# Kernel optimization log

Measured on AMD Instinct MI355X. Metric: run time of the kernel, lower is better.

The kernel has to match this reference:

```python
import jax, jax.numpy as jnp
import numpy as np

K = 128
HEADS = 8

def setup_inputs() -> dict:
    key = jax.random.key(0)
    ks = jax.random.split(key, 6)
    B, S = 4, 2048
    x = jax.random.normal(ks[0], (B, S, K), dtype=jnp.float32)
    sc = 1.0 / np.sqrt(K)
    Wq = jax.random.normal(ks[1], (K, K * HEADS), dtype=jnp.float32) * sc
    Wk = jax.random.normal(ks[2], (K, K * HEADS), dtype=jnp.float32) * sc
    Wv = jax.random.normal(ks[3], (K, K * HEADS), dtype=jnp.float32) * sc
    Wo = jax.random.normal(ks[4], (HEADS * K, K), dtype=jnp.float32) * (1.0 / np.sqrt(HEADS * K))
    bo = jnp.zeros((K,), dtype=jnp.float32)
    return {"x": x, "Wq": Wq, "Wk": Wk, "Wv": Wv, "Wo": Wo, "bo": bo}

def reference(x, Wq, Wk, Wv, Wo, bo):
    B, S, k = x.shape
    h = HEADS
    # projections: (B,S,k) @ (k, k*h) -> (B,S,h,k) -> (B,h,S,k)
    q = (x @ Wq).reshape(B, S, h, k).transpose(0, 2, 1, 3)
    kk = (x @ Wk).reshape(B, S, h, k).transpose(0, 2, 1, 3)
    v = (x @ Wv).reshape(B, S, h, k).transpose(0, 2, 1, 3)
    scale = k ** -0.25
    q = q * scale
    kk = kk * scale
    scores = jnp.einsum('bhqd,bhkd->bhqk', q, kk)  # (B,h,S,S)
    attn = jax.nn.softmax(scores, axis=-1)
    out = jnp.einsum('bhqk,bhkd->bhqd', attn, v)  # (B,h,S,k)
    out = out.transpose(0, 2, 1, 3).reshape(B, S, h * k)
    return out @ Wo + bo
```

## Files before the change

### kernel.cpp

```cpp
#include <hip/hip_runtime.h>


typedef __attribute__((ext_vector_type(8))) short bf16x8;
typedef __attribute__((ext_vector_type(4))) float f32x4;
typedef __attribute__((ext_vector_type(16))) float f32x16;
typedef __attribute__((ext_vector_type(4))) int i32x4;

#define LOG2E 1.4426950408889634f

__device__ __forceinline__ unsigned short f2bf(float f) {
  unsigned u = __builtin_bit_cast(unsigned, f);
  return (unsigned short)((u + 0x7fffu + ((u >> 16) & 1u)) >> 16);
}

__device__ __forceinline__ unsigned cvtpk(float lo, float hi) {
  unsigned r;
  asm("v_cvt_pk_bf16_f32 %0, %1, %2" : "=v"(r) : "v"(lo), "v"(hi));
  return r;
}

__device__ __forceinline__ float vexp2(float x) {
  float r;
  asm("v_exp_f32 %0, %1" : "=v"(r) : "v"(x));
  return r;
}

__global__ void prep_kernel(const float* __restrict__ x, const float* __restrict__ Wq,
                            const float* __restrict__ Wk, const float* __restrict__ Wv,
                            const float* __restrict__ Wo,
                            unsigned short* __restrict__ xb, unsigned short* __restrict__ Wtq,
                            unsigned short* __restrict__ Wtk, unsigned short* __restrict__ Wtv,
                            unsigned short* __restrict__ Wot) {
  int tid = blockIdx.x * 256 + threadIdx.x;
  if (tid < 8192 * 128) xb[tid] = f2bf(x[tid]);
  if (tid < 1024 * 128) {
    int r = tid >> 7, c = tid & 127;
    Wtq[tid] = f2bf(Wq[c * 1024 + r]);
    Wtk[tid] = f2bf(Wk[c * 1024 + r]);
    Wtv[tid] = f2bf(Wv[c * 1024 + r]);
    int r2 = tid >> 10, c2 = tid & 1023;
    Wot[tid] = f2bf(Wo[c2 * 128 + r2]);
  }
}

__device__ __forceinline__ void prefetch8(f32x4* r, const unsigned short* gsrc, int t) {
#pragma unroll
  for (int it = 0; it < 8; ++it) {
    int c = t + it * 256, row = c >> 4, col = c & 15;
    r[it] = *(const f32x4*)(gsrc + row * 128 + col * 8);
  }
}

__device__ __forceinline__ void write8(unsigned short* dst, const f32x4* r, int t) {
#pragma unroll
  for (int it = 0; it < 8; ++it) {
    int c = t + it * 256, row = c >> 4, col = c & 15;
    *(f32x4*)((char*)dst + row * 256 + ((col * 16) ^ ((row & 7) << 4))) = r[it];
  }
}

__device__ __forceinline__ void stage_128x128(unsigned short* dst, const unsigned short* gsrc, int t) {
#pragma unroll
  for (int it = 0; it < 8; ++it) {
    int c = t + it * 256, row = c >> 4, col = c & 15;
    *(f32x4*)((char*)dst + row * 256 + ((col * 16) ^ ((row & 7) << 4))) =
        *(const f32x4*)(gsrc + row * 128 + col * 8);
  }
}

__device__ __forceinline__ void mma128(const unsigned short* As, const unsigned short* Bs,
                                       int wm, int wn, int l, f32x4 acc[4][4]) {
  int lc = l & 15, kg = l >> 4;
#pragma unroll
  for (int kc = 0; kc < 4; ++kc) {
    bf16x8 a[4], b[4];
#pragma unroll
    for (int mi = 0; mi < 4; ++mi) {
      int ar = wm * 64 + mi * 16 + lc;
      a[mi] = *(const bf16x8*)((const char*)As + ar * 256 + ((kc * 64 + kg * 16) ^ ((ar & 7) << 4)));
    }
#pragma unroll
    for (int ni = 0; ni < 4; ++ni) {
      int br = wn * 64 + ni * 16 + lc;
      b[ni] = *(const bf16x8*)((const char*)Bs + br * 256 + ((kc * 64 + kg * 16) ^ ((br & 7) << 4)));
    }
#pragma unroll
    for (int mi = 0; mi < 4; ++mi)
#pragma unroll
      for (int ni = 0; ni < 4; ++ni)
        acc[mi][ni] = __builtin_amdgcn_mfma_f32_16x16x32_bf16(a[mi], b[ni], acc[mi][ni], 0, 0, 0);
  }
}

__global__ __launch_bounds__(256, 2) void qkv_kernel(const unsigned short* __restrict__ xb,
    const unsigned short* __restrict__ Wtq, const unsigned short* __restrict__ Wtk,
    const unsigned short* __restrict__ Wtv,
    unsigned short* __restrict__ Qb, unsigned short* __restrict__ Kb,
    unsigned short* __restrict__ Vt) {
  __shared__ unsigned short Xs[128 * 128], Ws[128 * 128];
  int m0 = blockIdx.x * 128, n0 = blockIdx.y * 128;
  int t = threadIdx.x, w = t >> 6, l = t & 63;
  int wm = w & 1, wn = w >> 1, lc = l & 15, kg = l >> 4;
  stage_128x128(Xs, xb + m0 * 128, t);
  stage_128x128(Ws, Wtq + n0 * 128, t);
  __syncthreads();

  f32x4 rw[8];
  prefetch8(rw, Wtk + n0 * 128, t);

  f32x4 acc[4][4];
#pragma unroll
  for (int mi = 0; mi < 4; ++mi)
#pragma unroll
    for (int ni = 0; ni < 4; ++ni) acc[mi][ni] = (f32x4){0.f, 0.f, 0.f, 0.f};
  mma128(Xs, Ws, wm, wn, l, acc);
  const float qscale = 0.29730177875068026f * LOG2E;
#pragma unroll
  for (int mi = 0; mi < 4; ++mi)
#pragma unroll
    for (int ni = 0; ni < 4; ++ni)
#pragma unroll
      for (int e = 0; e < 4; ++e) {
        int m = m0 + wm * 64 + mi * 16 + kg * 4 + e;
        int n = n0 + wn * 64 + ni * 16 + lc;
        int b = m >> 11, s = m & 2047, h = n >> 7, d = n & 127;
        Qb[((b * 8 + h) * 2048 + s) * 128 + d] = f2bf(acc[mi][ni][e] * qscale);
      }
  __syncthreads();
  write8(Ws, rw, t);
  __syncthreads();
  prefetch8(rw, Wtv + n0 * 128, t);

#pragma unroll
  for (int mi = 0; mi < 4; ++mi)
#pragma unroll
    for (int ni = 0; ni < 4; ++ni) acc[mi][ni] = (f32x4){0.f, 0.f, 0.f, 0.f};
  mma128(Xs, Ws, wm, wn, l, acc);
  const float kscale = 0.29730177875068026f;
#pragma unroll
  for (int mi = 0; mi < 4; ++mi)
#pragma unroll
    for (int ni = 0; ni < 4; ++ni)
#pragma unroll
      for (int e = 0; e < 4; ++e) {
        int m = m0 + wm * 64 + mi * 16 + kg * 4 + e;
        int n = n0 + wn * 64 + ni * 16 + lc;
        int b = m >> 11, s = m & 2047, h = n >> 7, d = n & 127;
        Kb[((b * 8 + h) * 2048 + s) * 128 + d] = f2bf(acc[mi][ni][e] * kscale);
      }
  __syncthreads();
  write8(Ws, rw, t);
  __syncthreads();

#pragma unroll
  for (int mi = 0; mi < 4; ++mi)
#pragma unroll
    for (int ni = 0; ni < 4; ++ni) acc[mi][ni] = (f32x4){0.f, 0.f, 0.f, 0.f};
  mma128(Ws, Xs, wm, wn, l, acc);
#pragma unroll
  for (int mi = 0; mi < 4; ++mi)
#pragma unroll
    for (int ni = 0; ni < 4; ++ni)
#pragma unroll
      for (int e = 0; e < 4; ++e) {
        int n = n0 + wm * 64 + mi * 16 + kg * 4 + e;
        int m = m0 + wn * 64 + ni * 16 + lc;
        int b = m >> 11, s = m & 2047, h = n >> 7, d = n & 127;
        Vt[((b * 8 + h) * 128 + d) * 2048 + s] = f2bf(acc[mi][ni][e]);
      }
}

__global__ __launch_bounds__(256, 2) void attn_kernel(const unsigned short* __restrict__ Qb,
    const unsigned short* __restrict__ Kb, const unsigned short* __restrict__ Vt,
    unsigned short* __restrict__ att) {
  __shared__ unsigned short lds[2][16384];
  int bid = blockIdx.x;
  int fid = (bid & 7) * 64 + (bid >> 3);
  int bh = fid >> 4, qt = fid & 15;
  const unsigned short* Qp = Qb + bh * 2048 * 128;
  const unsigned short* Kp = Kb + bh * 2048 * 128;
  const unsigned short* Vp = Vt + bh * 128 * 2048;
  int t = threadIdx.x, w = t >> 6, l = t & 63, lc = l & 31, hi = l >> 5;
  int q0 = qt * 128 + w * 32;

  bf16x8 qf[8];
  {
    const unsigned short* qr_ = Qp + (q0 + lc) * 128 + hi * 8;
#pragma unroll
    for (int kc = 0; kc < 8; ++kc) qf[kc] = *(const bf16x8*)(qr_ + kc * 16);
  }

  int kcol = l & 15, vc = l & 7;
  int krow[4], vrow[4];
#pragma unroll
  for (int i = 0; i < 4; ++i) { krow[i] = w * 16 + i * 4 + (l >> 4); vrow[i] = w * 32 + i * 8 + (l >> 3); }

  f32x16 acc[4];
#pragma unroll
  for (int i = 0; i < 4; ++i)
#pragma unroll
    for (int j = 0; j < 16; ++j) acc[i][j] = 0.f;
  float m_run = -1e30f, l_run = 0.f;

  f32x4 sk[4], sv[4];
#pragma unroll
  for (int i = 0; i < 4; ++i) {
    sk[i] = *(const f32x4*)(Kp + krow[i] * 128 + kcol * 8);
    sv[i] = *(const f32x4*)(Vp + vrow[i] * 2048 + vc * 8);
  }
#pragma unroll
  for (int i = 0; i < 4; ++i) {
    *(f32x4*)((char*)&lds[0][0] + krow[i] * 256 + ((kcol * 16) ^ ((krow[i] & 7) << 4))) = sk[i];
    *(f32x4*)((char*)&lds[0][8192] + vrow[i] * 128 + ((vc * 16) ^ ((vrow[i] & 7) << 4))) = sv[i];
  }
  __syncthreads();

  for (int kt = 0; kt < 32; ++kt) {
    int cur = kt & 1;
    if (kt < 31) {
      int kv0 = (kt + 1) * 64;
#pragma unroll
      for (int i = 0; i < 4; ++i) {
        sk[i] = *(const f32x4*)(Kp + (kv0 + krow[i]) * 128 + kcol * 8);
        sv[i] = *(const f32x4*)(Vp + vrow[i] * 2048 + kv0 + vc * 8);
      }
    }
    const char* Kb_ = (const char*)&lds[cur][0];
    const char* Vb_ = (const char*)&lds[cur][8192];

    f32x16 s0, s1;
#pragma unroll
    for (int j = 0; j < 16; ++j) { s0[j] = 0.f; s1[j] = 0.f; }
    __builtin_amdgcn_s_setprio(1);
#pragma unroll
    for (int kc = 0; kc < 8; ++kc) {
      int cb = kc * 32 + hi * 16;
      int r1 = 32 + lc;
      bf16x8 k0 = *(const bf16x8*)(Kb_ + lc * 256 + (cb ^ ((lc & 7) << 4)));
      bf16x8 k1 = *(const bf16x8*)(Kb_ + r1 * 256 + (cb ^ ((r1 & 7) << 4)));
      s0 = __builtin_amdgcn_mfma_f32_32x32x16_bf16(k0, qf[kc], s0, 0, 0, 0);
      s1 = __builtin_amdgcn_mfma_f32_32x32x16_bf16(k1, qf[kc], s1, 0, 0, 0);
    }
    __builtin_amdgcn_s_setprio(0);

    float t8[8];
#pragma unroll
    for (int j = 0; j < 8; ++j)
      t8[j] = fmaxf(fmaxf(s0[j], s0[j + 8]), fmaxf(s1[j], s1[j + 8]));
    float pmax = fmaxf(fmaxf(fmaxf(t8[0], t8[1]), fmaxf(t8[2], t8[3])),
                       fmaxf(fmaxf(t8[4], t8[5]), fmaxf(t8[6], t8[7])));
    pmax = fmaxf(pmax, __shfl_xor(pmax, 32));
    float mold = m_run;
    bool defer = (__all(pmax <= m_run + 11.5416f) != 0);
    if (!defer) m_run = fmaxf(m_run, pmax);
#pragma unroll
    for (int j = 0; j < 16; ++j) s0[j] = vexp2(s0[j] - m_run);
#pragma unroll
    for (int j = 0; j < 16; ++j) s1[j] = vexp2(s1[j] - m_run);
    float q8[8];
#pragma unroll
    for (int j = 0; j < 8; ++j)
      q8[j] = (s0[j] + s0[j + 8]) + (s1[j] + s1[j + 8]);
    float rs = ((q8[0] + q8[1]) + (q8[2] + q8[3])) + ((q8[4] + q8[5]) + (q8[6] + q8[7]));
    rs += __shfl_xor(rs, 32);
    if (!defer) {
      float resc = vexp2(mold - m_run);
      l_run = l_run * resc + rs;
#pragma unroll
      for (int r = 0; r < 16; ++r) {
        int qr = (r & 3) + 8 * (r >> 2) + 4 * hi;
        float f = __shfl(resc, qr, 32);
#pragma unroll
        for (int dt = 0; dt < 4; ++dt) acc[dt][r] *= f;
      }
    } else {
      l_run += rs;
    }

    bf16x8 pa[4];
#define PACK(ks, SX, o) { \
      unsigned x1 = cvtpk(SX[o], SX[(o) + 1]); \
      unsigned y1 = cvtpk(SX[(o) + 4], SX[(o) + 5]); \
      unsigned x2 = cvtpk(SX[(o) + 2], SX[(o) + 3]); \
      unsigned y2 = cvtpk(SX[(o) + 6], SX[(o) + 7]); \
      asm("v_permlane32_swap_b32 %0, %1" : "+v"(x1), "+v"(y1)); \
      asm("v_permlane32_swap_b32 %0, %1" : "+v"(x2), "+v"(y2)); \
      i32x4 pp; \
      pp[0] = (int)x1; pp[1] = (int)x2; pp[2] = (int)y1; pp[3] = (int)y2; \
      pa[ks] = __builtin_bit_cast(bf16x8, pp); }
    PACK(0, s0, 0) PACK(1, s0, 8) PACK(2, s1, 0) PACK(3, s1, 8)
#undef PACK

    __builtin_amdgcn_s_setprio(1);
#pragma unroll
    for (int ks = 0; ks < 4; ++ks) {
      int cb = ks * 32 + hi * 16;
#pragma unroll
      for (int dt = 0; dt < 4; ++dt) {
        int vr = dt * 32 + lc;
        bf16x8 vb = *(const bf16x8*)(Vb_ + vr * 128 + (cb ^ ((vr & 7) << 4)));
        acc[dt] = __builtin_amdgcn_mfma_f32_32x32x16_bf16(pa[ks], vb, acc[dt], 0, 0, 0);
      }
    }
    __builtin_amdgcn_s_setprio(0);

    if (kt < 31) {
      char* Kn = (char*)&lds[cur ^ 1][0];
      char* Vn = (char*)&lds[cur ^ 1][8192];
#pragma unroll
      for (int i = 0; i < 4; ++i) {
        *(f32x4*)(Kn + krow[i] * 256 + ((kcol * 16) ^ ((krow[i] & 7) << 4))) = sk[i];
        *(f32x4*)(Vn + vrow[i] * 128 + ((vc * 16) ^ ((vrow[i] & 7) << 4))) = sv[i];
      }
    }
    __syncthreads();
  }

  int b = bh >> 3, h = bh & 7;
#pragma unroll
  for (int r = 0; r < 16; ++r) {
    int qr = (r & 3) + 8 * (r >> 2) + 4 * hi;
    float linv = 1.f / __shfl(l_run, qr, 32);
    unsigned short* orow = att + ((b * 2048 + (q0 + qr)) * 8 + h) * 128 + lc;
#pragma unroll
    for (int dt = 0; dt < 4; ++dt) orow[dt * 32] = f2bf(acc[dt][r] * linv);
  }
}

__device__ __forceinline__ void mfma_64x64(const unsigned short* As, const unsigned short* Bs,
                                           int w, int l, f32x4 acc[4]) {
  int lc = l & 15, kg = l >> 4;
#pragma unroll
  for (int kc = 0; kc < 4; ++kc) {
    int ar = w * 16 + lc;
    bf16x8 a = *(const bf16x8*)((const char*)As + ar * 256 + ((kc * 64 + kg * 16) ^ ((ar & 7) << 4)));
#pragma unroll
    for (int tt = 0; tt < 4; ++tt) {
      int br = tt * 16 + lc;
      bf16x8 b = *(const bf16x8*)((const char*)Bs + br * 256 + ((kc * 64 + kg * 16) ^ ((br & 7) << 4)));
      acc[tt] = __builtin_amdgcn_mfma_f32_16x16x32_bf16(a, b, acc[tt], 0, 0, 0);
    }
  }
}

__global__ __launch_bounds__(256) void out_proj_kernel(const unsigned short* __restrict__ att,
    const unsigned short* __restrict__ Wot, const float* __restrict__ bo,
    float* __restrict__ out) {
  __shared__ unsigned short As[64 * 128], Bs[64 * 128];
  int m0 = blockIdx.x * 64, n0 = blockIdx.y * 64;
  int t = threadIdx.x, w = t >> 6, l = t & 63, lc = l & 15, kg = l >> 4;
  f32x4 acc[4];
#pragma unroll
  for (int i = 0; i < 4; ++i) acc[i] = (f32x4){0.f, 0.f, 0.f, 0.f};
  f32x4 ra[4], rb[4];
#pragma unroll
  for (int it = 0; it < 4; ++it) {
    int c = t + it * 256, row = c >> 4, col = c & 15;
    ra[it] = *(const f32x4*)(att + (m0 + row) * 1024 + col * 8);
    rb[it] = *(const f32x4*)(Wot + (n0 + row) * 1024 + col * 8);
  }
  for (int kt = 0; kt < 8; ++kt) {
    if (kt) __syncthreads();
#pragma unroll
    for (int it = 0; it < 4; ++it) {
      int c = t + it * 256, row = c >> 4, col = c & 15;
      *(f32x4*)((char*)As + row * 256 + ((col * 16) ^ ((row & 7) << 4))) = ra[it];
      *(f32x4*)((char*)Bs + row * 256 + ((col * 16) ^ ((row & 7) << 4))) = rb[it];
    }
    __syncthreads();
    if (kt < 7) {
#pragma unroll
      for (int it = 0; it < 4; ++it) {
        int c = t + it * 256, row = c >> 4, col = c & 15;
        ra[it] = *(const f32x4*)(att + (m0 + row) * 1024 + (kt + 1) * 128 + col * 8);
        rb[it] = *(const f32x4*)(Wot + (n0 + row) * 1024 + (kt + 1) * 128 + col * 8);
      }
    }
    mfma_64x64(As, Bs, w, l, acc);
  }
#pragma unroll
  for (int tt = 0; tt < 4; ++tt)
#pragma unroll
    for (int e = 0; e < 4; ++e) {
      int m = m0 + w * 16 + kg * 4 + e;
      int n = n0 + tt * 16 + lc;
      out[m * 128 + n] = acc[tt][e] + bo[n];
    }
}

extern "C" void kernel_launch(void* const* d_in, const int* in_sizes, int n_in,
                              void* d_out, int out_size, void* d_ws, size_t ws_size,
                              hipStream_t stream) {
  const float* x  = (const float*)d_in[0];
  const float* Wq = (const float*)d_in[1];
  const float* Wk = (const float*)d_in[2];
  const float* Wv = (const float*)d_in[3];
  const float* Wo = (const float*)d_in[4];
  const float* bo = (const float*)d_in[5];
  float* out = (float*)d_out;
  char* ws = (char*)d_ws;
  unsigned short* xb  = (unsigned short*)(ws);
  unsigned short* Wtq = (unsigned short*)(ws + (2u << 20));
  unsigned short* Wtk = (unsigned short*)(ws + (2u << 20) + (256u << 10));
  unsigned short* Wtv = (unsigned short*)(ws + (2u << 20) + (512u << 10));
  unsigned short* Wot = (unsigned short*)(ws + (2u << 20) + (768u << 10));
  unsigned short* Qb  = (unsigned short*)(ws + (3u << 20));
  unsigned short* Kb  = (unsigned short*)(ws + (3u << 20) + (16u << 20));
  unsigned short* Vt  = (unsigned short*)(ws + (3u << 20) + (32u << 20));
  unsigned short* att = (unsigned short*)(ws + (3u << 20) + (48u << 20));

  hipLaunchKernelGGL(prep_kernel, dim3(4096), dim3(256), 0, stream,
                     x, Wq, Wk, Wv, Wo, xb, Wtq, Wtk, Wtv, Wot);
  hipLaunchKernelGGL(qkv_kernel, dim3(64, 8), dim3(256), 0, stream,
                     xb, Wtq, Wtk, Wtv, Qb, Kb, Vt);
  hipLaunchKernelGGL(attn_kernel, dim3(512), dim3(256), 0, stream,
                     Qb, Kb, Vt, att);
  hipLaunchKernelGGL(out_proj_kernel, dim3(128, 2), dim3(256), 0, stream,
                     att, Wot, bo, out);
}
```

Baseline: 175.8 us.

## Software-pipeline QK^T one tile ahead in attention and vectorize prep transposes

```diff
diff --git a/kernel.cpp b/kernel.cpp
--- a/kernel.cpp
+++ b/kernel.cpp
@@ -25,22 +25,50 @@
   return r;
 }
 
-__global__ void prep_kernel(const float* __restrict__ x, const float* __restrict__ Wq,
-                            const float* __restrict__ Wk, const float* __restrict__ Wv,
-                            const float* __restrict__ Wo,
-                            unsigned short* __restrict__ xb, unsigned short* __restrict__ Wtq,
-                            unsigned short* __restrict__ Wtk, unsigned short* __restrict__ Wtv,
-                            unsigned short* __restrict__ Wot) {
-  int tid = blockIdx.x * 256 + threadIdx.x;
-  if (tid < 8192 * 128) xb[tid] = f2bf(x[tid]);
-  if (tid < 1024 * 128) {
-    int r = tid >> 7, c = tid & 127;
-    Wtq[tid] = f2bf(Wq[c * 1024 + r]);
-    Wtk[tid] = f2bf(Wk[c * 1024 + r]);
-    Wtv[tid] = f2bf(Wv[c * 1024 + r]);
-    int r2 = tid >> 10, c2 = tid & 1023;
-    Wot[tid] = f2bf(Wo[c2 * 128 + r2]);
-  }
+__global__ __launch_bounds__(256) void prep_kernel(const float* __restrict__ x,
+    const float* __restrict__ Wq, const float* __restrict__ Wk, const float* __restrict__ Wv,
+    const float* __restrict__ Wo,
+    unsigned short* __restrict__ xb, unsigned short* __restrict__ Wtq,
+    unsigned short* __restrict__ Wtk, unsigned short* __restrict__ Wtv,
+    unsigned short* __restrict__ Wot) {
+  __shared__ float tl[64][68];
+  int bid = blockIdx.x, t = threadIdx.x;
+  if (bid < 512) {
+    int idx = (bid * 256 + t) * 8;
+    f32x4 a = *(const f32x4*)(x + idx);
+    f32x4 b = *(const f32x4*)(x + idx + 4);
+    i32x4 o;
+    o[0] = (int)cvtpk(a[0], a[1]); o[1] = (int)cvtpk(a[2], a[3]);
+    o[2] = (int)cvtpk(b[0], b[1]); o[3] = (int)cvtpk(b[2], b[3]);
+    *(i32x4*)(xb + idx) = o;
+    return;
+  }
+  int tb = bid - 512;
+  int which = tb >> 5, tile = tb & 31;
+  const float* in; unsigned short* out; int K, N, kt_, nt_;
+  if (which == 0)      { in = Wq; out = Wtq; }
+  else if (which == 1) { in = Wk; out = Wtk; }
+  else if (which == 2) { in = Wv; out = Wtv; }
+  else                 { in = Wo; out = Wot; }
+  if (which < 3) { K = 128;  N = 1024; kt_ = tile >> 4; nt_ = tile & 15; }
+  else           { K = 1024; N = 128;  kt_ = tile >> 1; nt_ = tile & 1; }
+  int k0 = kt_ * 64, n0 = nt_ * 64;
+  int tr = t >> 4, tc = (t & 15) * 4;
+#pragma unroll
+  for (int i = 0; i < 4; ++i) {
+    f32x4 v = *(const f32x4*)(in + (k0 + tr + i * 16) * N + n0 + tc);
+#pragma unroll
+    for (int j = 0; j < 4; ++j) tl[tc + j][tr + i * 16] = v[j];
+  }
+  __syncthreads();
+  int n = t >> 2, c0 = (t & 3) * 16;
+  i32x4 o1, o2;
+#pragma unroll
+  for (int j = 0; j < 4; ++j) o1[j] = (int)cvtpk(tl[n][c0 + 2 * j], tl[n][c0 + 2 * j + 1]);
+#pragma unroll
+  for (int j = 0; j < 4; ++j) o2[j] = (int)cvtpk(tl[n][c0 + 8 + 2 * j], tl[n][c0 + 9 + 2 * j]);
+  *(i32x4*)(out + (n0 + n) * K + k0 + c0) = o1;
+  *(i32x4*)(out + (n0 + n) * K + k0 + c0 + 8) = o2;
 }
 
 __device__ __forceinline__ void prefetch8(f32x4* r, const unsigned short* gsrc, int t) {
@@ -168,6 +196,21 @@
         int b = m >> 11, s = m & 2047, h = n >> 7, d = n & 127;
         Vt[((b * 8 + h) * 128 + d) * 2048 + s] = f2bf(acc[mi][ni][e]);
       }
+}
+
+__device__ __forceinline__ void qk_step(const char* Kb_, const bf16x8* qf, int lc, int hi,
+                                        f32x16& s0, f32x16& s1) {
+#pragma unroll
+  for (int j = 0; j < 16; ++j) { s0[j] = 0.f; s1[j] = 0.f; }
+  int r1 = 32 + lc;
+#pragma unroll
+  for (int kc = 0; kc < 8; ++kc) {
+    int cb = kc * 32 + hi * 16;
+    bf16x8 k0 = *(const bf16x8*)(Kb_ + lc * 256 + (cb ^ ((lc & 7) << 4)));
+    bf16x8 k1 = *(const bf16x8*)(Kb_ + r1 * 256 + (cb ^ ((r1 & 7) << 4)));
+    s0 = __builtin_amdgcn_mfma_f32_32x32x16_bf16(k0, qf[kc], s0, 0, 0, 0);
+    s1 = __builtin_amdgcn_mfma_f32_32x32x16_bf16(k1, qf[kc], s1, 0, 0, 0);
+  }
 }
 
 __global__ __launch_bounds__(256, 2) void attn_kernel(const unsigned short* __restrict__ Qb,
@@ -213,35 +256,17 @@
     *(f32x4*)((char*)&lds[0][0] + krow[i] * 256 + ((kcol * 16) ^ ((krow[i] & 7) << 4))) = sk[i];
     *(f32x4*)((char*)&lds[0][8192] + vrow[i] * 128 + ((vc * 16) ^ ((vrow[i] & 7) << 4))) = sv[i];
   }
-  __syncthreads();
+#pragma unroll
+  for (int i = 0; i < 4; ++i) {
+    sk[i] = *(const f32x4*)(Kp + (64 + krow[i]) * 128 + kcol * 8);
+    sv[i] = *(const f32x4*)(Vp + vrow[i] * 2048 + 64 + vc * 8);
+  }
+  __syncthreads();
+  f32x16 s0, s1;
+  qk_step((const char*)&lds[0][0], qf, lc, hi, s0, s1);
 
   for (int kt = 0; kt < 32; ++kt) {
-    int cur = kt & 1;
-    if (kt < 31) {
-      int kv0 = (kt + 1) * 64;
-#pragma unroll
-      for (int i = 0; i < 4; ++i) {
-        sk[i] = *(const f32x4*)(Kp + (kv0 + krow[i]) * 128 + kcol * 8);
-        sv[i] = *(const f32x4*)(Vp + vrow[i] * 2048 + kv0 + vc * 8);
-      }
-    }
-    const char* Kb_ = (const char*)&lds[cur][0];
-    const char* Vb_ = (const char*)&lds[cur][8192];
-
-    f32x16 s0, s1;
-#pragma unroll
-    for (int j = 0; j < 16; ++j) { s0[j] = 0.f; s1[j] = 0.f; }
-    __builtin_amdgcn_s_setprio(1);
-#pragma unroll
-    for (int kc = 0; kc < 8; ++kc) {
-      int cb = kc * 32 + hi * 16;
-      int r1 = 32 + lc;
-      bf16x8 k0 = *(const bf16x8*)(Kb_ + lc * 256 + (cb ^ ((lc & 7) << 4)));
-      bf16x8 k1 = *(const bf16x8*)(Kb_ + r1 * 256 + (cb ^ ((r1 & 7) << 4)));
-      s0 = __builtin_amdgcn_mfma_f32_32x32x16_bf16(k0, qf[kc], s0, 0, 0, 0);
-      s1 = __builtin_amdgcn_mfma_f32_32x32x16_bf16(k1, qf[kc], s1, 0, 0, 0);
-    }
-    __builtin_amdgcn_s_setprio(0);
+    int nb = (kt + 1) & 1;
 
     float t8[8];
 #pragma unroll
@@ -291,7 +316,29 @@
     PACK(0, s0, 0) PACK(1, s0, 8) PACK(2, s1, 0) PACK(3, s1, 8)
 #undef PACK
 
+    __syncthreads();
+    if (kt < 31) {
+      char* Kn = (char*)&lds[nb][0];
+      char* Vn = (char*)&lds[nb][8192];
+#pragma unroll
+      for (int i = 0; i < 4; ++i) {
+        *(f32x4*)(Kn + krow[i] * 256 + ((kcol * 16) ^ ((krow[i] & 7) << 4))) = sk[i];
+        *(f32x4*)(Vn + vrow[i] * 128 + ((vc * 16) ^ ((vrow[i] & 7) << 4))) = sv[i];
+      }
+      if (kt < 30) {
+        int kv0 = (kt + 2) * 64;
+#pragma unroll
+        for (int i = 0; i < 4; ++i) {
+          sk[i] = *(const f32x4*)(Kp + (kv0 + krow[i]) * 128 + kcol * 8);
+          sv[i] = *(const f32x4*)(Vp + vrow[i] * 2048 + kv0 + vc * 8);
+        }
+      }
+    }
+    __syncthreads();
+
     __builtin_amdgcn_s_setprio(1);
+    if (kt < 31) qk_step((const char*)&lds[nb][0], qf, lc, hi, s0, s1);
+    const char* Vb_ = (const char*)&lds[kt & 1][8192];
 #pragma unroll
     for (int ks = 0; ks < 4; ++ks) {
       int cb = ks * 32 + hi * 16;
@@ -303,17 +350,6 @@
       }
     }
     __builtin_amdgcn_s_setprio(0);
-
-    if (kt < 31) {
-      char* Kn = (char*)&lds[cur ^ 1][0];
-      char* Vn = (char*)&lds[cur ^ 1][8192];
-#pragma unroll
-      for (int i = 0; i < 4; ++i) {
-        *(f32x4*)(Kn + krow[i] * 256 + ((kcol * 16) ^ ((krow[i] & 7) << 4))) = sk[i];
-        *(f32x4*)(Vn + vrow[i] * 128 + ((vc * 16) ^ ((vrow[i] & 7) << 4))) = sv[i];
-      }
-    }
-    __syncthreads();
   }
 
   int b = bh >> 3, h = bh & 7;
@@ -409,7 +445,7 @@
   unsigned short* Vt  = (unsigned short*)(ws + (3u << 20) + (32u << 20));
   unsigned short* att = (unsigned short*)(ws + (3u << 20) + (48u << 20));
 
-  hipLaunchKernelGGL(prep_kernel, dim3(4096), dim3(256), 0, stream,
+  hipLaunchKernelGGL(prep_kernel, dim3(640), dim3(256), 0, stream,
                      x, Wq, Wk, Wv, Wo, xb, Wtq, Wtk, Wtv, Wot);
   hipLaunchKernelGGL(qkv_kernel, dim3(64, 8), dim3(256), 0, stream,
                      xb, Wtq, Wtk, Wtv, Qb, Kb, Vt);
```

Result: faster. 167.1 us (-5.0%).
